# Optimization experiments

Hardware: AMD Instinct MI355X
Metric: run time of the kernel (lower is better)

## Reference

```python
import jax, jax.numpy as jnp
import numpy as np

B, K = 2048, 256
ED = RD = HD = 256
AD = ED + RD          # action_dim = 512
IN = ED + HD + RD     # 768
NUM_E, NUM_R = 100000, 500
HUGE = jnp.float32(1e31)  # ops.HUGE_INT


def setup_inputs() -> dict:
    key = jax.random.key(0)
    ks = jax.random.split(key, 12)
    s = 0.05  # keep logits in a sane range
    E = jax.random.normal(ks[0], (B, ED), jnp.float32)
    H = jax.random.normal(ks[1], (B, HD), jnp.float32)
    Q = jax.random.normal(ks[2], (B, RD), jnp.float32)
    W1 = jax.random.normal(ks[3], (AD, IN), jnp.float32) * s
    b1 = jnp.zeros((AD,), jnp.float32)
    W2 = jax.random.normal(ks[4], (AD, AD), jnp.float32) * s
    b2 = jnp.zeros((AD,), jnp.float32)
    emb_r = jax.random.normal(ks[5], (NUM_R, RD), jnp.float32) * s
    emb_e = jax.random.normal(ks[6], (NUM_E, ED), jnp.float32) * s
    # binary action mask (variable-size action spaces, padded); col 0 always valid
    action_mask = (jax.random.uniform(ks[7], (B, K)) > 0.3).astype(jnp.float32)
    action_mask = action_mask.at[:, 0].set(1.0)
    r_space = jax.random.randint(ks[8], (B, K), 0, NUM_R)
    e_space = jax.random.randint(ks[9], (B, K), 0, NUM_E)
    return {"E": E, "H": H, "Q": Q, "W1": W1, "b1": b1, "W2": W2, "b2": b2,
            "emb_r": emb_r, "emb_e": emb_e, "action_mask": action_mask,
            "r_space": r_space, "e_space": e_space}


def reference(E, H, Q, W1, b1, W2, b2, emb_r, emb_e, action_mask, r_space, e_space):
    # state MLP: X = W2Dropout(W2(relu(W1(cat([E, H, Q])))))  (dropout = identity at eval)
    X = jnp.concatenate([E, H, Q], axis=-1)           # [B, IN]
    X = jax.nn.relu(X @ W1.T + b1)                    # [B, AD]
    X2 = X @ W2.T + b2                                # [B, AD]
    # gather action embeddings: A = cat([emb_r[r], emb_e[e]])  [B, K, AD]
    A = jnp.concatenate([emb_r[r_space], emb_e[e_space]], axis=-1)
    # masked softmax over action space
    scores = jnp.einsum('bkd,bd->bk', A, X2) - (1.0 - action_mask) * HUGE
    action_dist = jax.nn.softmax(scores, axis=-1)     # [B, K]
    entropy = -jnp.sum(action_dist * jnp.log(action_dist + 1e-20), axis=-1)  # [B]
    return action_dist, entropy
```

## Files before the change

kernel.cpp:

```cpp
#include <hip/hip_runtime.h>
#include <hip/hip_bf16.h>
#include <math.h>

#define B_   2048
#define K_   256
#define AD_  512
#define IN_  768
#define NR_  500
#define NRP_ 512
#define NE_  100000

typedef __attribute__((ext_vector_type(8))) short short8;
typedef __attribute__((ext_vector_type(4))) float float4v;

__device__ __forceinline__ unsigned short f2bf(float f) {
    unsigned int u = __float_as_uint(f);
    unsigned int r = u + 0x7FFF + ((u >> 16) & 1);
    return (unsigned short)(r >> 16);
}
__device__ __forceinline__ float bf2f(short s) {
    return __uint_as_float(((unsigned int)(unsigned short)s) << 16);
}

#define EE_N4 (NE_ * 256 / 4)
#define X_N4  (B_ * IN_ / 4)
#define W1_N4 (AD_ * IN_ / 4)
#define W2_N4 (AD_ * AD_ / 4)
#define ER_N4 (NR_ * 256 / 4)
#define PREP_TOTAL (EE_N4 + X_N4 + W1_N4 + W2_N4 + ER_N4)
__global__ __launch_bounds__(256) void prep_kernel(
    const float* __restrict__ E, const float* __restrict__ H,
    const float* __restrict__ Q, const float* __restrict__ W1,
    const float* __restrict__ W2, const float* __restrict__ emb_r,
    const float* __restrict__ emb_e,
    ushort* __restrict__ Xb, ushort* __restrict__ W1b,
    ushort* __restrict__ W2b, ushort* __restrict__ emb_rb,
    ushort* __restrict__ emb_eb)
{
    int t = blockIdx.x * 256 + threadIdx.x;
    const float* src; ushort* dst; int off;
    if (t < EE_N4) { src = emb_e; dst = emb_eb; off = t; }
    else {
        t -= EE_N4;
        if (t < X_N4) {
            const int base = t * 4;
            const int row = base / IN_, col = base % IN_;
            src = (col < 256) ? &E[row * 256 + col]
                : (col < 512) ? &H[row * 256 + col - 256]
                              : &Q[row * 256 + col - 512];
            const float4 v = *(const float4*)src;
            ushort4 o;
            o.x = f2bf(v.x); o.y = f2bf(v.y); o.z = f2bf(v.z); o.w = f2bf(v.w);
            *(ushort4*)&Xb[base] = o;
            return;
        }
        t -= X_N4;
        if (t < W1_N4)                 { src = W1;    dst = W1b;    off = t; }
        else if (t < W1_N4 + W2_N4)    { src = W2;    dst = W2b;    off = t - W1_N4; }
        else if (t < W1_N4 + W2_N4 + ER_N4) { src = emb_r; dst = emb_rb; off = t - W1_N4 - W2_N4; }
        else return;
    }
    const float4 v = *(const float4*)&src[(size_t)off * 4];
    ushort4 o;
    o.x = f2bf(v.x); o.y = f2bf(v.y); o.z = f2bf(v.z); o.w = f2bf(v.w);
    *(ushort4*)&dst[(size_t)off * 4] = o;
}

template<int K, bool RELU, bool OUT_BF16, bool BIAS, bool EMIT_RHALF>
__global__ __launch_bounds__(256) void gemm_bf16_kernel(
    const ushort* __restrict__ A, const ushort* __restrict__ Bw,
    const float* __restrict__ bias, ushort* __restrict__ outb,
    float* __restrict__ outf, ushort* __restrict__ rhalf)
{
    constexpr int PITCH = 72;
    __shared__ ushort Asl[2][64 * PITCH];
    __shared__ ushort Bsl[2][64 * PITCH];
    const int tid = threadIdx.x;
    const int lane = tid & 63, w = tid >> 6;
    const int n0 = blockIdx.x * 64, m0 = blockIdx.y * 64;
    const int lrow = tid >> 2, lcg = (tid & 3) * 16;
    const int q = lane >> 4, l16 = lane & 15;

    const ushort* aptr = &A[(size_t)(m0 + lrow) * K + lcg];
    const ushort* bptr = &Bw[(size_t)(n0 + lrow) * K + lcg];

    short8 ra0 = *(const short8*)aptr;
    short8 ra1 = *(const short8*)(aptr + 8);
    short8 rb0 = *(const short8*)bptr;
    short8 rb1 = *(const short8*)(bptr + 8);
    *(short8*)&Asl[0][lrow * PITCH + lcg]     = ra0;
    *(short8*)&Asl[0][lrow * PITCH + lcg + 8] = ra1;
    *(short8*)&Bsl[0][lrow * PITCH + lcg]     = rb0;
    *(short8*)&Bsl[0][lrow * PITCH + lcg + 8] = rb1;

    float4v acc[4] = {};
    int buf = 0;
    __syncthreads();
    for (int k0 = 0; k0 < K; k0 += 64) {
        if (k0 + 64 < K) {
            ra0 = *(const short8*)(aptr + k0 + 64);
            ra1 = *(const short8*)(aptr + k0 + 64 + 8);
            rb0 = *(const short8*)(bptr + k0 + 64);
            rb1 = *(const short8*)(bptr + k0 + 64 + 8);
        }
        #pragma unroll
        for (int kh = 0; kh < 64; kh += 32) {
            const short8 af = *(const short8*)&Asl[buf][(w * 16 + l16) * PITCH + kh + q * 8];
            #pragma unroll
            for (int jn = 0; jn < 4; ++jn) {
                const short8 bfr = *(const short8*)&Bsl[buf][(jn * 16 + l16) * PITCH + kh + q * 8];
                acc[jn] = __builtin_amdgcn_mfma_f32_16x16x32_bf16(af, bfr, acc[jn], 0, 0, 0);
            }
        }
        if (k0 + 64 < K) {
            *(short8*)&Asl[buf ^ 1][lrow * PITCH + lcg]     = ra0;
            *(short8*)&Asl[buf ^ 1][lrow * PITCH + lcg + 8] = ra1;
            *(short8*)&Bsl[buf ^ 1][lrow * PITCH + lcg]     = rb0;
            *(short8*)&Bsl[buf ^ 1][lrow * PITCH + lcg + 8] = rb1;
            __syncthreads();
            buf ^= 1;
        }
    }
    #pragma unroll
    for (int jn = 0; jn < 4; ++jn) {
        const int n = n0 + jn * 16 + l16;
        const float bn = BIAS ? bias[n] : 0.0f;
        #pragma unroll
        for (int r = 0; r < 4; ++r) {
            const int m = m0 + w * 16 + q * 4 + r;
            float c = acc[jn][r] + bn;
            if (RELU) c = fmaxf(c, 0.0f);
            if (OUT_BF16) outb[(size_t)m * AD_ + n] = f2bf(c);
            else          outf[(size_t)m * AD_ + n] = c;
            if (EMIT_RHALF && n < 256) rhalf[(size_t)m * 256 + n] = f2bf(c);
        }
    }
}

__global__ __launch_bounds__(256) void scores_kernel(
    const float* __restrict__ X2, const float* __restrict__ R,
    const ushort* __restrict__ emb_eb, const float* __restrict__ mask,
    const int* __restrict__ r_space, const int* __restrict__ e_space,
    float* __restrict__ dist, float* __restrict__ entropy)
{
    const int b = blockIdx.x;
    const int tid = threadIdx.x;
    const int lane = tid & 63, wid = tid >> 6;
    const int half = lane >> 5, l32 = lane & 31;

    __shared__ int   s_e[K_];
    __shared__ float s_dot[K_];
    __shared__ float s_red[12];

    s_e[tid] = e_space[b * K_ + tid];
    const int   r_mine = r_space[b * K_ + tid];
    const float mk     = mask[b * K_ + tid];
    const float bias   = R[(size_t)b * NRP_ + r_mine] - (1.0f - mk) * 1e31f;
    const float4 x0 = *(const float4*)&X2[(size_t)b * AD_ + 256 + l32 * 8];
    const float4 x1 = *(const float4*)&X2[(size_t)b * AD_ + 256 + l32 * 8 + 4];
    __syncthreads();

    const int kbase = wid * 64;
    #pragma unroll
    for (int kk = 0; kk < 64; kk += 16) {
        float p[8];
        #pragma unroll
        for (int u = 0; u < 8; ++u) {
            const int row = kbase + kk + u * 2 + half;
            const int e = s_e[row];
            const short8 ae = *(const short8*)&emb_eb[(size_t)e * 256 + l32 * 8];
            p[u] = bf2f(ae[0]) * x0.x + bf2f(ae[1]) * x0.y
                 + bf2f(ae[2]) * x0.z + bf2f(ae[3]) * x0.w
                 + bf2f(ae[4]) * x1.x + bf2f(ae[5]) * x1.y
                 + bf2f(ae[6]) * x1.z + bf2f(ae[7]) * x1.w;
        }
        #pragma unroll
        for (int off = 16; off >= 1; off >>= 1) {
            #pragma unroll
            for (int u = 0; u < 8; ++u) p[u] += __shfl_down(p[u], off, 32);
        }
        if (l32 == 0) {
            #pragma unroll
            for (int u = 0; u < 8; ++u) s_dot[kbase + kk + u * 2 + half] = p[u];
        }
    }
    __syncthreads();

    const float v = s_dot[tid] + bias;

    float m = v;
    #pragma unroll
    for (int off = 32; off >= 1; off >>= 1) m = fmaxf(m, __shfl_down(m, off));
    if (lane == 0) s_red[wid] = m;
    __syncthreads();
    if (tid == 0)
        s_red[8] = fmaxf(fmaxf(s_red[0], s_red[1]), fmaxf(s_red[2], s_red[3]));
    __syncthreads();
    const float bmax = s_red[8];

    const float ev = __expf(v - bmax);
    float s = ev;
    float t = ev * (v - bmax);
    #pragma unroll
    for (int off = 32; off >= 1; off >>= 1) {
        s += __shfl_down(s, off);
        t += __shfl_down(t, off);
    }
    if (lane == 0) { s_red[wid] = s; s_red[4 + wid] = t; }
    __syncthreads();
    if (tid == 0) {
        s_red[9]  = s_red[0] + s_red[1] + s_red[2] + s_red[3];
        s_red[10] = s_red[4] + s_red[5] + s_red[6] + s_red[7];
    }
    __syncthreads();
    const float ssum = s_red[9];

    dist[(size_t)b * K_ + tid] = ev / ssum;
    if (tid == 0)
        entropy[b] = logf(ssum) - s_red[10] / ssum;
}

extern "C" void kernel_launch(void* const* d_in, const int* in_sizes, int n_in,
                              void* d_out, int out_size, void* d_ws, size_t ws_size,
                              hipStream_t stream) {
    const float* E     = (const float*)d_in[0];
    const float* H     = (const float*)d_in[1];
    const float* Q     = (const float*)d_in[2];
    const float* W1    = (const float*)d_in[3];
    const float* b1    = (const float*)d_in[4];
    const float* W2    = (const float*)d_in[5];
    const float* b2    = (const float*)d_in[6];
    const float* emb_r = (const float*)d_in[7];
    const float* emb_e = (const float*)d_in[8];
    const float* mask  = (const float*)d_in[9];
    const int* r_space = (const int*)d_in[10];
    const int* e_space = (const int*)d_in[11];

    float* out_dist = (float*)d_out;
    float* out_ent  = out_dist + (size_t)B_ * K_;

    char* ws = (char*)d_ws;
    ushort* Xb     = (ushort*)ws;  ws += (size_t)B_ * IN_ * 2;
    ushort* W1b    = (ushort*)ws;  ws += (size_t)AD_ * IN_ * 2;
    ushort* W2b    = (ushort*)ws;  ws += (size_t)AD_ * AD_ * 2;
    ushort* emb_rb = (ushort*)ws;  ws += (size_t)NRP_ * 256 * 2;
    ushort* emb_eb = (ushort*)ws;  ws += (size_t)NE_ * 256 * 2;
    ushort* H1b    = (ushort*)ws;  ws += (size_t)B_ * AD_ * 2;
    float*  X2     = (float*)ws;   ws += (size_t)B_ * AD_ * 4;
    ushort* X2rb   = (ushort*)ws;  ws += (size_t)B_ * 256 * 2;
    float*  Rt     = (float*)ws;   ws += (size_t)B_ * NRP_ * 4;

    prep_kernel<<<(PREP_TOTAL + 255) / 256, 256, 0, stream>>>(
        E, H, Q, W1, W2, emb_r, emb_e, Xb, W1b, W2b, emb_rb, emb_eb);

    dim3 g(AD_ / 64, B_ / 64);
    gemm_bf16_kernel<IN_, true,  true,  true,  false><<<g, 256, 0, stream>>>(
        Xb, W1b, b1, H1b, nullptr, nullptr);
    gemm_bf16_kernel<AD_, false, false, true,  true ><<<g, 256, 0, stream>>>(
        H1b, W2b, b2, nullptr, X2, X2rb);
    gemm_bf16_kernel<256, false, false, false, false><<<dim3(NRP_ / 64, B_ / 64), 256, 0, stream>>>(
        X2rb, emb_rb, nullptr, nullptr, Rt, nullptr);

    scores_kernel<<<B_, 256, 0, stream>>>(X2, Rt, emb_eb, mask,
                                          r_space, e_space, out_dist, out_ent);
}
```

Before: 242.3 us.

## Overlap emb_e bf16 cast with GEMM launches via extra cast blocks

```diff
diff --git a/kernel.cpp b/kernel.cpp
--- a/kernel.cpp
+++ b/kernel.cpp
@@ -22,44 +22,38 @@
     return __uint_as_float(((unsigned int)(unsigned short)s) << 16);
 }
 
-#define EE_N4 (NE_ * 256 / 4)
 #define X_N4  (B_ * IN_ / 4)
 #define W1_N4 (AD_ * IN_ / 4)
 #define W2_N4 (AD_ * AD_ / 4)
 #define ER_N4 (NR_ * 256 / 4)
-#define PREP_TOTAL (EE_N4 + X_N4 + W1_N4 + W2_N4 + ER_N4)
-__global__ __launch_bounds__(256) void prep_kernel(
+#define EE_N4 (NE_ * 256 / 4)
+#define PREP1_TOTAL (X_N4 + W1_N4 + W2_N4 + ER_N4)
+__global__ __launch_bounds__(256) void prep1_kernel(
     const float* __restrict__ E, const float* __restrict__ H,
     const float* __restrict__ Q, const float* __restrict__ W1,
     const float* __restrict__ W2, const float* __restrict__ emb_r,
-    const float* __restrict__ emb_e,
     ushort* __restrict__ Xb, ushort* __restrict__ W1b,
-    ushort* __restrict__ W2b, ushort* __restrict__ emb_rb,
-    ushort* __restrict__ emb_eb)
+    ushort* __restrict__ W2b, ushort* __restrict__ emb_rb)
 {
     int t = blockIdx.x * 256 + threadIdx.x;
     const float* src; ushort* dst; int off;
-    if (t < EE_N4) { src = emb_e; dst = emb_eb; off = t; }
-    else {
-        t -= EE_N4;
-        if (t < X_N4) {
-            const int base = t * 4;
-            const int row = base / IN_, col = base % IN_;
-            src = (col < 256) ? &E[row * 256 + col]
-                : (col < 512) ? &H[row * 256 + col - 256]
-                              : &Q[row * 256 + col - 512];
-            const float4 v = *(const float4*)src;
-            ushort4 o;
-            o.x = f2bf(v.x); o.y = f2bf(v.y); o.z = f2bf(v.z); o.w = f2bf(v.w);
-            *(ushort4*)&Xb[base] = o;
-            return;
-        }
-        t -= X_N4;
-        if (t < W1_N4)                 { src = W1;    dst = W1b;    off = t; }
-        else if (t < W1_N4 + W2_N4)    { src = W2;    dst = W2b;    off = t - W1_N4; }
-        else if (t < W1_N4 + W2_N4 + ER_N4) { src = emb_r; dst = emb_rb; off = t - W1_N4 - W2_N4; }
-        else return;
-    }
+    if (t < X_N4) {
+        const int base = t * 4;
+        const int row = base / IN_, col = base % IN_;
+        src = (col < 256) ? &E[row * 256 + col]
+            : (col < 512) ? &H[row * 256 + col - 256]
+                          : &Q[row * 256 + col - 512];
+        const float4 v = *(const float4*)src;
+        ushort4 o;
+        o.x = f2bf(v.x); o.y = f2bf(v.y); o.z = f2bf(v.z); o.w = f2bf(v.w);
+        *(ushort4*)&Xb[base] = o;
+        return;
+    }
+    t -= X_N4;
+    if (t < W1_N4)                 { src = W1;    dst = W1b;    off = t; }
+    else if (t < W1_N4 + W2_N4)    { src = W2;    dst = W2b;    off = t - W1_N4; }
+    else if (t < W1_N4 + W2_N4 + ER_N4) { src = emb_r; dst = emb_rb; off = t - W1_N4 - W2_N4; }
+    else return;
     const float4 v = *(const float4*)&src[(size_t)off * 4];
     ushort4 o;
     o.x = f2bf(v.x); o.y = f2bf(v.y); o.z = f2bf(v.z); o.w = f2bf(v.w);
@@ -67,17 +61,36 @@
 }
 
 template<int K, bool RELU, bool OUT_BF16, bool BIAS, bool EMIT_RHALF>
-__global__ __launch_bounds__(256) void gemm_bf16_kernel(
+__global__ __launch_bounds__(256) void gemm_fused_kernel(
     const ushort* __restrict__ A, const ushort* __restrict__ Bw,
     const float* __restrict__ bias, ushort* __restrict__ outb,
-    float* __restrict__ outf, ushort* __restrict__ rhalf)
+    float* __restrict__ outf, ushort* __restrict__ rhalf,
+    const float* __restrict__ castsrc, ushort* __restrict__ castdst,
+    long cast_base, long cast_end)
 {
     constexpr int PITCH = 72;
     __shared__ ushort Asl[2][64 * PITCH];
     __shared__ ushort Bsl[2][64 * PITCH];
+    const int bid = blockIdx.x;
     const int tid = threadIdx.x;
+
+    if (bid >= 256) {
+        const int cb = bid - 256;
+        long i4 = cast_base + (long)cb * 1024 + tid;
+        #pragma unroll
+        for (int it = 0; it < 4; ++it, i4 += 256) {
+            if (i4 < cast_end) {
+                const float4 v = *(const float4*)&castsrc[i4 * 4];
+                ushort4 o;
+                o.x = f2bf(v.x); o.y = f2bf(v.y); o.z = f2bf(v.z); o.w = f2bf(v.w);
+                *(ushort4*)&castdst[i4 * 4] = o;
+            }
+        }
+        return;
+    }
+
     const int lane = tid & 63, w = tid >> 6;
-    const int n0 = blockIdx.x * 64, m0 = blockIdx.y * 64;
+    const int n0 = (bid & 7) * 64, m0 = (bid >> 3) * 64;
     const int lrow = tid >> 2, lcg = (tid & 3) * 16;
     const int q = lane >> 4, l16 = lane & 15;
 
@@ -131,7 +144,7 @@
             float c = acc[jn][r] + bn;
             if (RELU) c = fmaxf(c, 0.0f);
             if (OUT_BF16) outb[(size_t)m * AD_ + n] = f2bf(c);
-            else          outf[(size_t)m * AD_ + n] = c;
+            else if (!EMIT_RHALF || n >= 256) outf[(size_t)m * AD_ + n] = c;
             if (EMIT_RHALF && n < 256) rhalf[(size_t)m * 256 + n] = f2bf(c);
         }
     }
@@ -168,7 +181,8 @@
         for (int u = 0; u < 8; ++u) {
             const int row = kbase + kk + u * 2 + half;
             const int e = s_e[row];
-            const short8 ae = *(const short8*)&emb_eb[(size_t)e * 256 + l32 * 8];
+            const short8 ae = __builtin_nontemporal_load(
+                (const short8*)&emb_eb[(size_t)e * 256 + l32 * 8]);
             p[u] = bf2f(ae[0]) * x0.x + bf2f(ae[1]) * x0.y
                  + bf2f(ae[2]) * x0.z + bf2f(ae[3]) * x0.w
                  + bf2f(ae[4]) * x1.x + bf2f(ae[5]) * x1.y
@@ -250,16 +264,22 @@
     ushort* X2rb   = (ushort*)ws;  ws += (size_t)B_ * 256 * 2;
     float*  Rt     = (float*)ws;   ws += (size_t)B_ * NRP_ * 4;
 
-    prep_kernel<<<(PREP_TOTAL + 255) / 256, 256, 0, stream>>>(
-        E, H, Q, W1, W2, emb_r, emb_e, Xb, W1b, W2b, emb_rb, emb_eb);
-
-    dim3 g(AD_ / 64, B_ / 64);
-    gemm_bf16_kernel<IN_, true,  true,  true,  false><<<g, 256, 0, stream>>>(
-        Xb, W1b, b1, H1b, nullptr, nullptr);
-    gemm_bf16_kernel<AD_, false, false, true,  true ><<<g, 256, 0, stream>>>(
-        H1b, W2b, b2, nullptr, X2, X2rb);
-    gemm_bf16_kernel<256, false, false, false, false><<<dim3(NRP_ / 64, B_ / 64), 256, 0, stream>>>(
-        X2rb, emb_rb, nullptr, nullptr, Rt, nullptr);
+    prep1_kernel<<<(PREP1_TOTAL + 255) / 256, 256, 0, stream>>>(
+        E, H, Q, W1, W2, emb_r, Xb, W1b, W2b, emb_rb);
+
+    const long chunk = (EE_N4 + 2) / 3;
+    const int  cast_blocks = (int)((chunk + 1023) / 1024);
+    const int  grid = 256 + cast_blocks;
+
+    gemm_fused_kernel<IN_, true,  true,  true,  false><<<grid, 256, 0, stream>>>(
+        Xb, W1b, b1, H1b, nullptr, nullptr,
+        emb_e, emb_eb, 0L, chunk);
+    gemm_fused_kernel<AD_, false, false, true,  true ><<<grid, 256, 0, stream>>>(
+        H1b, W2b, b2, nullptr, X2, X2rb,
+        emb_e, emb_eb, chunk, 2 * chunk);
+    gemm_fused_kernel<256, false, false, false, false><<<grid, 256, 0, stream>>>(
+        X2rb, emb_rb, nullptr, nullptr, Rt, nullptr,
+        emb_e, emb_eb, 2 * chunk, (long)EE_N4);
 
     scores_kernel<<<B_, 256, 0, stream>>>(X2, Rt, emb_eb, mask,
                                           r_space, e_space, out_dist, out_ent);
```

Measured after the change: 247.5 us. 2.1% more time.
